# Kernel tuning notes

Measured on AMD Instinct MI355X. Metric: run time of the kernel, lower is better.

The kernel has to match this reference:

```python
import jax, jax.numpy as jnp
import numpy as np

EPS = 1e-5
NH, NP = 12, 4  # heads, points per level


def _ln(x, g, b):
    m = x.mean(-1, keepdims=True)
    v = x.var(-1, keepdims=True)
    return (x - m) / jnp.sqrt(v + EPS) * g + b


def _bilinear(v, g, H_, W_):
    # v: [B, nh, H_*W_, d] flattened feature map; g: [B, nh, Lq, np, 2] normalized locs in [0,1]
    # torch grid_sample(align_corners=False, padding='zeros') with grid = 2*loc-1 => pixel = loc*W - 0.5
    x = g[..., 0] * W_ - 0.5
    y = g[..., 1] * H_ - 0.5
    x0 = jnp.floor(x)
    y0 = jnp.floor(y)
    wx1 = x - x0
    wy1 = y - y0
    wx0 = 1.0 - wx1
    wy0 = 1.0 - wy1
    d = v.shape[-1]
    Bn, nh, Lq, np_ = x.shape
    out = jnp.zeros((Bn, nh, Lq, np_, d), v.dtype)
    for xi, yi, w in ((x0, y0, wx0 * wy0), (x0 + 1, y0, wx1 * wy0),
                      (x0, y0 + 1, wx0 * wy1), (x0 + 1, y0 + 1, wx1 * wy1)):
        valid = (xi >= 0) & (xi < W_) & (yi >= 0) & (yi < H_)
        xc = jnp.clip(xi, 0, W_ - 1).astype(jnp.int32)
        yc = jnp.clip(yi, 0, H_ - 1).astype(jnp.int32)
        idx = (yc * W_ + xc).reshape(Bn, nh, Lq * np_, 1)
        gv = jnp.take_along_axis(v, idx, axis=2).reshape(Bn, nh, Lq, np_, d)
        out = out + (w * valid.astype(v.dtype))[..., None] * gv
    return out


def setup_inputs() -> dict:
    key = jax.random.key(0)
    ks = jax.random.split(key, 16)
    B, Lq, C = 4, 4096, 768
    nl = 1
    Hs = Ws = 64
    Lin = Hs * Ws
    hid = int(C * 0.25)
    s = 0.02
    f32 = jnp.float32
    return {
        'query': jax.random.normal(ks[0], (B, Lq, C), f32),
        'reference_points': jax.random.uniform(ks[1], (B, Lq, nl, 2), f32),
        'feat': jax.random.normal(ks[2], (B, Lin, C), f32),
        'spatial_shapes': np.array([[Hs, Ws]], dtype=np.int64),
        'level_start_index': np.array([0], dtype=np.int64),
        'H': Hs, 'W': Ws,
        'qn_g': jnp.ones(C, f32), 'qn_b': jnp.zeros(C, f32),
        'fn_g': jnp.ones(C, f32), 'fn_b': jnp.zeros(C, f32),
        'Wv': jax.random.normal(ks[3], (C, C), f32) * s, 'bv': jnp.zeros(C, f32),
        'Woff': jax.random.normal(ks[4], (C, NH * nl * NP * 2), f32) * s,
        'boff': jax.random.normal(ks[5], (NH * nl * NP * 2,), f32) * 0.1,
        'Watt': jax.random.normal(ks[6], (C, NH * nl * NP), f32) * s,
        'batt': jnp.zeros(NH * nl * NP, f32),
        'Wout': jax.random.normal(ks[7], (C, C), f32) * s, 'bout': jnp.zeros(C, f32),
        'ffn_g': jnp.ones(C, f32), 'ffn_b': jnp.zeros(C, f32),
        'W1': jax.random.normal(ks[8], (C, hid), f32) * s, 'b1': jnp.zeros(hid, f32),
        'W2': jax.random.normal(ks[9], (hid, C), f32) * s, 'b2': jnp.zeros(C, f32),
    }


def reference(query, reference_points, feat, spatial_shapes, level_start_index, H, W,
              qn_g, qn_b, fn_g, fn_b, Wv, bv, Woff, boff, Watt, batt, Wout, bout,
              ffn_g, ffn_b, W1, b1, W2, b2):
    B, Lq, C = query.shape
    nl = spatial_shapes.shape[0]
    d = C // NH
    qn = _ln(query, qn_g, qn_b)
    fn = _ln(feat, fn_g, fn_b)
    value = (fn @ Wv + bv).reshape(B, -1, NH, d)
    off = (qn @ Woff + boff).reshape(B, Lq, NH, nl, NP, 2)
    attw = jax.nn.softmax((qn @ Watt + batt).reshape(B, Lq, NH, nl * NP), axis=-1)
    attw = attw.reshape(B, Lq, NH, nl, NP)
    # offset normalizer is [W_l, H_l]
    norm = np.stack([spatial_shapes[:, 1], spatial_shapes[:, 0]], -1).astype(np.float32)
    loc = reference_points[:, :, None, :, None, :] + off / jnp.asarray(norm)[None, None, None, :, None, :]
    out = jnp.zeros((B, NH, Lq, d), query.dtype)
    for l in range(nl):
        H_, W_ = int(spatial_shapes[l, 0]), int(spatial_shapes[l, 1])
        s0 = int(level_start_index[l])
        v = value[:, s0:s0 + H_ * W_].transpose(0, 2, 1, 3)       # [B, nh, HW, d]
        g = loc[:, :, :, l].transpose(0, 2, 1, 3, 4)              # [B, nh, Lq, np, 2]
        sampled = _bilinear(v, g, H_, W_)                         # [B, nh, Lq, np, d]
        w = attw[:, :, :, l].transpose(0, 2, 1, 3)                # [B, nh, Lq, np]
        out = out + jnp.sum(sampled * w[..., None], axis=3)
    attn = out.transpose(0, 2, 1, 3).reshape(B, Lq, C) @ Wout + bout
    query = query + attn
    h = _ln(query, ffn_g, ffn_b)
    h = jax.nn.gelu(h @ W1 + b1, approximate=False)
    return query + (h @ W2 + b2)
```

## Files before the change

### kernel.cpp

```cpp
#include <hip/hip_runtime.h>
#include <hip/hip_bf16.h>
#include <math.h>

#define B_    4
#define LQ    4096
#define CC    768
#define NH_   12
#define DH    64
#define NP_   4
#define HH    64
#define WW    64
#define HID   192
#define ROWS  (B_ * LQ)
#define EPS_  1e-5f

typedef __bf16 bf16x8 __attribute__((ext_vector_type(8)));
typedef __bf16 bf16x4 __attribute__((ext_vector_type(4)));
typedef float  f32x4  __attribute__((ext_vector_type(4)));

typedef __attribute__((address_space(3))) void* lds_vp;
typedef const __attribute__((address_space(1))) void* gbl_vp;

struct PrepJob { const float* W; __bf16* Wt; int K; int N; int Npad; };
struct PrepJobs { PrepJob j[6]; };

__global__ __launch_bounds__(256)
void prep_all(PrepJobs jobs) {
    PrepJob job = jobs.j[blockIdx.z];
    int k0 = blockIdx.x * 64, n0 = blockIdx.y * 64;
    if (k0 >= job.K || n0 >= job.Npad) return;
    __shared__ float tile[64][65];
    int c = threadIdx.x & 63, r0 = threadIdx.x >> 6;
    #pragma unroll
    for (int i = 0; i < 16; ++i) {
        int kk = i * 4 + r0;
        float v = 0.f;
        if (k0 + kk < job.K && n0 + c < job.N) v = job.W[(size_t)(k0 + kk) * job.N + n0 + c];
        tile[kk][c] = v;
    }
    __syncthreads();
    #pragma unroll
    for (int i = 0; i < 16; ++i) {
        int nn = i * 4 + r0;
        if (n0 + nn < job.Npad && k0 + c < job.K)
            job.Wt[(size_t)(n0 + nn) * job.K + k0 + c] = (__bf16)tile[c][nn];
    }
}

__inline__ __device__ float wave_sum64(float v) {
    #pragma unroll
    for (int o = 32; o > 0; o >>= 1) v += __shfl_down(v, o, 64);
    return v;
}

__global__ __launch_bounds__(256)
void ln2_kernel(const float* __restrict__ x0, const float* __restrict__ g0,
                const float* __restrict__ b0, __bf16* __restrict__ y0,
                const float* __restrict__ x1, const float* __restrict__ g1,
                const float* __restrict__ b1, __bf16* __restrict__ y1) {
    int sel = blockIdx.y;
    const float* x = sel ? x1 : x0;
    const float* g = sel ? g1 : g0;
    const float* b = sel ? b1 : b0;
    __bf16* y = sel ? y1 : y0;
    int row = blockIdx.x;
    const float* xr = x + (size_t)row * CC;
    __bf16* yr = y + (size_t)row * CC;
    int t = threadIdx.x;
    f32x4 xv = {0.f, 0.f, 0.f, 0.f};
    if (t < 192) xv = *(const f32x4*)(xr + t * 4);
    float s  = xv[0] + xv[1] + xv[2] + xv[3];
    float s2 = xv[0]*xv[0] + xv[1]*xv[1] + xv[2]*xv[2] + xv[3]*xv[3];
    __shared__ float red[8];
    float ws = wave_sum64(s), ws2 = wave_sum64(s2);
    int w = t >> 6;
    if ((t & 63) == 0) { red[w] = ws; red[4 + w] = ws2; }
    __syncthreads();
    float S  = red[0] + red[1] + red[2] + red[3];
    float S2 = red[4] + red[5] + red[6] + red[7];
    float mean = S / CC;
    float inv  = rsqrtf(S2 / CC - mean * mean + EPS_);
    if (t < 192) {
        f32x4 gv = *(const f32x4*)(g + t * 4);
        f32x4 bv = *(const f32x4*)(b + t * 4);
        bf16x4 o;
        #pragma unroll
        for (int e = 0; e < 4; ++e)
            o[e] = (__bf16)((xv[e] - mean) * inv * gv[e] + bv[e]);
        *(bf16x4*)(yr + t * 4) = o;
    }
}

__global__ __launch_bounds__(256)
void ln_bf_kernel(const __bf16* __restrict__ x, const float* __restrict__ g,
                  const float* __restrict__ b, __bf16* __restrict__ y) {
    int row = blockIdx.x;
    const __bf16* xr = x + (size_t)row * CC;
    __bf16* yr = y + (size_t)row * CC;
    int t = threadIdx.x;
    float xv[8]; bf16x8 raw = {};
    if (t < 96) raw = *(const bf16x8*)(xr + t * 8);
    float s = 0.f, s2 = 0.f;
    #pragma unroll
    for (int e = 0; e < 8; ++e) { xv[e] = (float)raw[e]; s += xv[e]; s2 += xv[e]*xv[e]; }
    __shared__ float red[8];
    float ws = wave_sum64(s), ws2 = wave_sum64(s2);
    int w = t >> 6;
    if ((t & 63) == 0) { red[w] = ws; red[4 + w] = ws2; }
    __syncthreads();
    float S  = red[0] + red[1] + red[2] + red[3];
    float S2 = red[4] + red[5] + red[6] + red[7];
    float mean = S / CC;
    float inv  = rsqrtf(S2 / CC - mean * mean + EPS_);
    if (t < 96) {
        bf16x8 o;
        #pragma unroll
        for (int e = 0; e < 8; ++e)
            o[e] = (__bf16)((xv[e] - mean) * inv * g[t * 8 + e] + b[t * 8 + e]);
        *(bf16x8*)(yr + t * 8) = o;
    }
}

__global__ __launch_bounds__(256, 8)
void gemm64(const __bf16* __restrict__ A, const __bf16* __restrict__ Bt,
            const float* __restrict__ ba, int Nsplit, const float* __restrict__ bb,
            const void* __restrict__ res, void* __restrict__ out,
            int M, int K, int N, int flags) {
    __shared__ __bf16 As[2][64 * 32];
    __shared__ __bf16 Bs[2][64 * 32];

    int t = threadIdx.x;
    int lane = t & 63, wave = t >> 6;

    int nwg = gridDim.x * gridDim.y;
    int bid = blockIdx.y * gridDim.x + blockIdx.x;
    int swz = (bid & 7) * (nwg >> 3) + (bid >> 3);
    int bx = swz % gridDim.x, by = swz / gridDim.x;
    int bm = by * 64, bn = bx * 64;

    f32x4 acc[4] = {};

    int row0 = t >> 2, kc0 = (t & 3) ^ ((row0 >> 1) & 3);
    const __bf16* a0 = A  + (size_t)(bm + row0) * K + kc0 * 8;
    const __bf16* b0 = Bt + (size_t)(bn + row0) * K + kc0 * 8;

    int rbase = wave * 16 + (lane & 15);
    int nbase = lane & 15;
    int kq = lane >> 4;

    #define STAGE(bi, kt) do {                                                                   \
        int koff_ = (kt) * 32;                                                                   \
        __builtin_amdgcn_global_load_lds((gbl_vp)(a0 + koff_), (lds_vp)&As[bi][t * 8], 16, 0, 0); \
        __builtin_amdgcn_global_load_lds((gbl_vp)(b0 + koff_), (lds_vp)&Bs[bi][t * 8], 16, 0, 0); \
    } while (0)

    #define COMPUTE(bi) do {                                                                     \
        bf16x8 afr = *(const bf16x8*)&As[bi][rbase * 32 + ((kq ^ ((rbase >> 1) & 3)) * 8)];      \
        _Pragma("unroll")                                                                        \
        for (int j = 0; j < 4; ++j) {                                                            \
            int n = nbase + j * 16;                                                              \
            bf16x8 bfr = *(const bf16x8*)&Bs[bi][n * 32 + ((kq ^ ((n >> 1) & 3)) * 8)];          \
            acc[j] = __builtin_amdgcn_mfma_f32_16x16x32_bf16(afr, bfr, acc[j], 0, 0, 0);         \
        }                                                                                        \
    } while (0)

    int nt = K >> 5;
    STAGE(0, 0);
    STAGE(1, 1);
    for (int tt = 0; tt < nt; ++tt) {
        int cur = tt & 1;
        if (tt < nt - 1) asm volatile("s_waitcnt vmcnt(2)\n\ts_barrier" ::: "memory");
        else             asm volatile("s_waitcnt vmcnt(0)\n\ts_barrier" ::: "memory");
        COMPUTE(cur);
        asm volatile("s_waitcnt lgkmcnt(0)\n\ts_barrier" ::: "memory");
        if (tt + 2 < nt) STAGE(cur, tt + 2);
    }

    #undef STAGE
    #undef COMPUTE

    int rowq = lane >> 4;
    int do_gelu = flags & 1, out_bf = flags & 2, res_bf = flags & 4;
    #pragma unroll
    for (int j = 0; j < 4; ++j) {
        int c = bn + j * 16 + (lane & 15);
        if (c < N) {
            float bias = (c < Nsplit) ? ba[c] : bb[c - Nsplit];
            #pragma unroll
            for (int r = 0; r < 4; ++r) {
                int m = bm + wave * 16 + rowq * 4 + r;
                float v = acc[j][r] + bias;
                if (do_gelu) v = 0.5f * v * (1.f + erff(v * 0.70710678118f));
                size_t oi = (size_t)m * N + c;
                if (res) v += res_bf ? (float)((const __bf16*)res)[oi]
                                     : ((const float*)res)[oi];
                if (out_bf) ((__bf16*)out)[oi] = (__bf16)v;
                else        ((float*)out)[oi]  = v;
            }
        }
    }
}

__global__ __launch_bounds__(256)
void sample_kernel(const __bf16* __restrict__ value, const float* __restrict__ offatt,
                   const float* __restrict__ refp, __bf16* __restrict__ out) {
    int wid  = blockIdx.x * 4 + (threadIdx.x >> 6);
    int lane = threadIdx.x & 63;
    int h  = wid % NH_;
    int bq = wid / NH_;
    int b  = bq / LQ;

    const float* oa = offatt + (size_t)bq * 144;
    float rx = refp[(size_t)bq * 2 + 0] * (float)WW - 0.5f;
    float ry = refp[(size_t)bq * 2 + 1] * (float)HH - 0.5f;

    float l0 = oa[96 + h * 4 + 0], l1 = oa[96 + h * 4 + 1];
    float l2 = oa[96 + h * 4 + 2], l3 = oa[96 + h * 4 + 3];
    float mx = fmaxf(fmaxf(l0, l1), fmaxf(l2, l3));
    float e0 = __expf(l0 - mx), e1 = __expf(l1 - mx);
    float e2 = __expf(l2 - mx), e3 = __expf(l3 - mx);
    float rs = 1.f / (e0 + e1 + e2 + e3);

    int pp = lane >> 4;
    int g  = lane & 15;
    float wpl = (pp == 0) ? e0 : (pp == 1) ? e1 : (pp == 2) ? e2 : e3;
    wpl *= rs;

    const float* oxy = oa + h * 8 + pp * 2;
    float x = rx + oxy[0];
    float y = ry + oxy[1];
    float x0f = floorf(x), y0f = floorf(y);
    float wx1 = x - x0f, wy1 = y - y0f;
    float wx0 = 1.f - wx1, wy0 = 1.f - wy1;
    int x0 = (int)x0f, y0 = (int)y0f;
    int x1 = x0 + 1, y1 = y0 + 1;
    float mx0 = ((unsigned)x0 < (unsigned)WW) ? wx0 : 0.f;
    float mx1 = ((unsigned)x1 < (unsigned)WW) ? wx1 : 0.f;
    float my0 = (((unsigned)y0 < (unsigned)HH) ? wy0 : 0.f) * wpl;
    float my1 = (((unsigned)y1 < (unsigned)HH) ? wy1 : 0.f) * wpl;
    int xc0 = x0 & (WW - 1), xc1 = x1 & (WW - 1);
    int r0 = (y0 & (HH - 1)) << 6, r1 = (y1 & (HH - 1)) << 6;

    const __bf16* vbase = value + (size_t)b * (LQ * CC) + h * DH + g * 4;
    bf16x4 v00 = *(const bf16x4*)(vbase + (size_t)(r0 + xc0) * CC);
    bf16x4 v01 = *(const bf16x4*)(vbase + (size_t)(r0 + xc1) * CC);
    bf16x4 v10 = *(const bf16x4*)(vbase + (size_t)(r1 + xc0) * CC);
    bf16x4 v11 = *(const bf16x4*)(vbase + (size_t)(r1 + xc1) * CC);
    float w00 = mx0 * my0, w01 = mx1 * my0, w10 = mx0 * my1, w11 = mx1 * my1;

    f32x4 acc;
    #pragma unroll
    for (int e = 0; e < 4; ++e)
        acc[e] = w00 * (float)v00[e] + w01 * (float)v01[e]
               + w10 * (float)v10[e] + w11 * (float)v11[e];

    #pragma unroll
    for (int e = 0; e < 4; ++e) {
        acc[e] += __shfl_xor(acc[e], 16, 64);
        acc[e] += __shfl_xor(acc[e], 32, 64);
    }
    if (pp == 0) {
        bf16x4 o;
        o[0] = (__bf16)acc[0]; o[1] = (__bf16)acc[1];
        o[2] = (__bf16)acc[2]; o[3] = (__bf16)acc[3];
        *(bf16x4*)(out + (size_t)bq * CC + h * DH + g * 4) = o;
    }
}

extern "C" void kernel_launch(void* const* d_in, const int* in_sizes, int n_in,
                              void* d_out, int out_size, void* d_ws, size_t ws_size,
                              hipStream_t stream) {
    const float* query = (const float*)d_in[0];
    const float* refp  = (const float*)d_in[1];
    const float* feat  = (const float*)d_in[2];
    const float* qn_g  = (const float*)d_in[7];
    const float* qn_b  = (const float*)d_in[8];
    const float* fn_g  = (const float*)d_in[9];
    const float* fn_b  = (const float*)d_in[10];
    const float* Wv    = (const float*)d_in[11];
    const float* bv    = (const float*)d_in[12];
    const float* Woff  = (const float*)d_in[13];
    const float* boff  = (const float*)d_in[14];
    const float* Watt  = (const float*)d_in[15];
    const float* batt  = (const float*)d_in[16];
    const float* Wout  = (const float*)d_in[17];
    const float* bout  = (const float*)d_in[18];
    const float* ffn_g = (const float*)d_in[19];
    const float* ffn_b = (const float*)d_in[20];
    const float* W1    = (const float*)d_in[21];
    const float* b1    = (const float*)d_in[22];
    const float* W2    = (const float*)d_in[23];
    const float* b2    = (const float*)d_in[24];
    float* out = (float*)d_out;

    char* ws = (char*)d_ws;
    __bf16* WvT    = (__bf16*)(ws + 0);
    __bf16* WcombT = (__bf16*)(ws + 1179648);
    __bf16* WoutT  = (__bf16*)(ws + 1572864);
    __bf16* W1T    = (__bf16*)(ws + 2752512);
    __bf16* W2T    = (__bf16*)(ws + 3145728);
    float*  offatt_f = (float*)(ws + 3670016);
    __bf16* h1_bf    = (__bf16*)offatt_f;
    __bf16* bufA     = (__bf16*)(ws + 13107200);
    __bf16* qn_bf    = bufA;
    __bf16* value_bf = bufA;
    __bf16* bufB     = (__bf16*)(ws + 38273024);
    __bf16* fn_bf    = bufB;
    __bf16* samp_bf  = bufB;
    __bf16* h_bf     = bufB;
    __bf16* attn_bf  = (__bf16*)(ws + 63438848);

    dim3 blk(256);

    PrepJobs jobs;
    jobs.j[0] = {Wv,   WvT,             768, 768, 768};
    jobs.j[1] = {Woff, WcombT,          768,  96,  96};
    jobs.j[2] = {Watt, WcombT + 96*768, 768,  48,  96};
    jobs.j[3] = {Wout, WoutT,           768, 768, 768};
    jobs.j[4] = {W1,   W1T,             768, 192, 192};
    jobs.j[5] = {W2,   W2T,             192, 768, 768};
    prep_all<<<dim3(12, 12, 6), blk, 0, stream>>>(jobs);

    ln2_kernel<<<dim3(ROWS, 2), blk, 0, stream>>>(query, qn_g, qn_b, qn_bf,
                                                  feat,  fn_g, fn_b, fn_bf);

    gemm64<<<dim3(3, ROWS / 64), blk, 0, stream>>>(
        qn_bf, WcombT, boff, 96, batt, nullptr, offatt_f, ROWS, CC, 144, 0);
    gemm64<<<dim3(12, ROWS / 64), blk, 0, stream>>>(
        fn_bf, WvT, bv, CC, nullptr, nullptr, value_bf, ROWS, CC, CC, 2);
    sample_kernel<<<ROWS * NH_ / 4, blk, 0, stream>>>(value_bf, offatt_f, refp, samp_bf);
    gemm64<<<dim3(12, ROWS / 64), blk, 0, stream>>>(
        samp_bf, WoutT, bout, CC, nullptr, query, attn_bf, ROWS, CC, CC, 2);
    ln_bf_kernel<<<ROWS, blk, 0, stream>>>(attn_bf, ffn_g, ffn_b, h_bf);
    gemm64<<<dim3(3, ROWS / 64), blk, 0, stream>>>(
        h_bf, W1T, b1, HID, nullptr, nullptr, h1_bf, ROWS, CC, HID, 1 | 2);
    gemm64<<<dim3(12, ROWS / 64), blk, 0, stream>>>(
        h1_bf, W2T, b2, CC, nullptr, attn_bf, out, ROWS, HID, CC, 4);
}
```

Measured before the change: 431.4 us.

## Replace LDS double-buffered GEMM with direct global-to-register MFMA operand loads

The GEMM no longer stages A and B tiles through shared memory with async global-to-LDS copies and barriers. Each wave now loads its MFMA fragments straight from global memory into registers, and the K loop is unrolled. This removes LDS traffic and barrier synchronisation. In exchange, the four waves each re-read the shared B tile from global memory or cache, the loads are strided 16-byte accesses per row, and the occupancy hint drops from 8 to 4 blocks.

```diff
diff --git a/kernel.cpp b/kernel.cpp
--- a/kernel.cpp
+++ b/kernel.cpp
@@ -17,9 +17,6 @@
 typedef __bf16 bf16x8 __attribute__((ext_vector_type(8)));
 typedef __bf16 bf16x4 __attribute__((ext_vector_type(4)));
 typedef float  f32x4  __attribute__((ext_vector_type(4)));
-
-typedef __attribute__((address_space(3))) void* lds_vp;
-typedef const __attribute__((address_space(1))) void* gbl_vp;
 
 struct PrepJob { const float* W; __bf16* Wt; int K; int N; int Npad; };
 struct PrepJobs { PrepJob j[6]; };
@@ -121,14 +118,11 @@
     }
 }
 
-__global__ __launch_bounds__(256, 8)
-void gemm64(const __bf16* __restrict__ A, const __bf16* __restrict__ Bt,
-            const float* __restrict__ ba, int Nsplit, const float* __restrict__ bb,
-            const void* __restrict__ res, void* __restrict__ out,
-            int M, int K, int N, int flags) {
-    __shared__ __bf16 As[2][64 * 32];
-    __shared__ __bf16 Bs[2][64 * 32];
-
+__global__ __launch_bounds__(256, 4)
+void gemm_reg(const __bf16* __restrict__ A, const __bf16* __restrict__ Bt,
+              const float* __restrict__ ba, int Nsplit, const float* __restrict__ bb,
+              const void* __restrict__ res, void* __restrict__ out,
+              int M, int K, int N, int flags) {
     int t = threadIdx.x;
     int lane = t & 63, wave = t >> 6;
 
@@ -138,52 +132,34 @@
     int bx = swz % gridDim.x, by = swz / gridDim.x;
     int bm = by * 64, bn = bx * 64;
 
+    int rsel = lane & 15, kq = lane >> 4;
+
+    const __bf16* pA  = A  + (size_t)(bm + wave * 16 + rsel) * K + kq * 8;
+    const __bf16* pB0 = Bt + (size_t)(bn + rsel)      * K + kq * 8;
+    const __bf16* pB1 = pB0 + (size_t)16 * K;
+    const __bf16* pB2 = pB0 + (size_t)32 * K;
+    const __bf16* pB3 = pB0 + (size_t)48 * K;
+
     f32x4 acc[4] = {};
 
-    int row0 = t >> 2, kc0 = (t & 3) ^ ((row0 >> 1) & 3);
-    const __bf16* a0 = A  + (size_t)(bm + row0) * K + kc0 * 8;
-    const __bf16* b0 = Bt + (size_t)(bn + row0) * K + kc0 * 8;
-
-    int rbase = wave * 16 + (lane & 15);
-    int nbase = lane & 15;
-    int kq = lane >> 4;
-
-    #define STAGE(bi, kt) do {                                                                   \
-        int koff_ = (kt) * 32;                                                                   \
-        __builtin_amdgcn_global_load_lds((gbl_vp)(a0 + koff_), (lds_vp)&As[bi][t * 8], 16, 0, 0); \
-        __builtin_amdgcn_global_load_lds((gbl_vp)(b0 + koff_), (lds_vp)&Bs[bi][t * 8], 16, 0, 0); \
-    } while (0)
-
-    #define COMPUTE(bi) do {                                                                     \
-        bf16x8 afr = *(const bf16x8*)&As[bi][rbase * 32 + ((kq ^ ((rbase >> 1) & 3)) * 8)];      \
-        _Pragma("unroll")                                                                        \
-        for (int j = 0; j < 4; ++j) {                                                            \
-            int n = nbase + j * 16;                                                              \
-            bf16x8 bfr = *(const bf16x8*)&Bs[bi][n * 32 + ((kq ^ ((n >> 1) & 3)) * 8)];          \
-            acc[j] = __builtin_amdgcn_mfma_f32_16x16x32_bf16(afr, bfr, acc[j], 0, 0, 0);         \
-        }                                                                                        \
-    } while (0)
-
-    int nt = K >> 5;
-    STAGE(0, 0);
-    STAGE(1, 1);
-    for (int tt = 0; tt < nt; ++tt) {
-        int cur = tt & 1;
-        if (tt < nt - 1) asm volatile("s_waitcnt vmcnt(2)\n\ts_barrier" ::: "memory");
-        else             asm volatile("s_waitcnt vmcnt(0)\n\ts_barrier" ::: "memory");
-        COMPUTE(cur);
-        asm volatile("s_waitcnt lgkmcnt(0)\n\ts_barrier" ::: "memory");
-        if (tt + 2 < nt) STAGE(cur, tt + 2);
-    }
-
-    #undef STAGE
-    #undef COMPUTE
+    #pragma unroll 6
+    for (int k0 = 0; k0 < K; k0 += 32) {
+        bf16x8 afr = *(const bf16x8*)(pA  + k0);
+        bf16x8 b0  = *(const bf16x8*)(pB0 + k0);
+        bf16x8 b1  = *(const bf16x8*)(pB1 + k0);
+        bf16x8 b2  = *(const bf16x8*)(pB2 + k0);
+        bf16x8 b3  = *(const bf16x8*)(pB3 + k0);
+        acc[0] = __builtin_amdgcn_mfma_f32_16x16x32_bf16(afr, b0, acc[0], 0, 0, 0);
+        acc[1] = __builtin_amdgcn_mfma_f32_16x16x32_bf16(afr, b1, acc[1], 0, 0, 0);
+        acc[2] = __builtin_amdgcn_mfma_f32_16x16x32_bf16(afr, b2, acc[2], 0, 0, 0);
+        acc[3] = __builtin_amdgcn_mfma_f32_16x16x32_bf16(afr, b3, acc[3], 0, 0, 0);
+    }
 
     int rowq = lane >> 4;
     int do_gelu = flags & 1, out_bf = flags & 2, res_bf = flags & 4;
     #pragma unroll
     for (int j = 0; j < 4; ++j) {
-        int c = bn + j * 16 + (lane & 15);
+        int c = bn + j * 16 + rsel;
         if (c < N) {
             float bias = (c < Nsplit) ? ba[c] : bb[c - Nsplit];
             #pragma unroll
@@ -324,16 +300,16 @@
     ln2_kernel<<<dim3(ROWS, 2), blk, 0, stream>>>(query, qn_g, qn_b, qn_bf,
                                                   feat,  fn_g, fn_b, fn_bf);
 
-    gemm64<<<dim3(3, ROWS / 64), blk, 0, stream>>>(
+    gemm_reg<<<dim3(3, ROWS / 64), blk, 0, stream>>>(
         qn_bf, WcombT, boff, 96, batt, nullptr, offatt_f, ROWS, CC, 144, 0);
-    gemm64<<<dim3(12, ROWS / 64), blk, 0, stream>>>(
+    gemm_reg<<<dim3(12, ROWS / 64), blk, 0, stream>>>(
         fn_bf, WvT, bv, CC, nullptr, nullptr, value_bf, ROWS, CC, CC, 2);
     sample_kernel<<<ROWS * NH_ / 4, blk, 0, stream>>>(value_bf, offatt_f, refp, samp_bf);
-    gemm64<<<dim3(12, ROWS / 64), blk, 0, stream>>>(
+    gemm_reg<<<dim3(12, ROWS / 64), blk, 0, stream>>>(
         samp_bf, WoutT, bout, CC, nullptr, query, attn_bf, ROWS, CC, CC, 2);
     ln_bf_kernel<<<ROWS, blk, 0, stream>>>(attn_bf, ffn_g, ffn_b, h_bf);
-    gemm64<<<dim3(3, ROWS / 64), blk, 0, stream>>>(
+    gemm_reg<<<dim3(3, ROWS / 64), blk, 0, stream>>>(
         h_bf, W1T, b1, HID, nullptr, nullptr, h1_bf, ROWS, CC, HID, 1 | 2);
-    gemm64<<<dim3(12, ROWS / 64), blk, 0, stream>>>(
+    gemm_reg<<<dim3(12, ROWS / 64), blk, 0, stream>>>(
         h1_bf, W2T, b2, CC, nullptr, attn_bf, out, ROWS, HID, CC, 4);
 }
```

Measured after the change: 736.8 us. +70.8%, slower.

## Add 256x256-tile GEMM kernel for the three wide N=768 projections

Applied to the files above, without the earlier changes.

Adds a 512-thread GEMM with 256x256 output tiles, 64-wide K steps, XOR-swizzled LDS layout and direct global-to-LDS loads. It replaces the 64x64-tile kernel for the value, output and second FFN projections. Larger tiles give more operand reuse per loaded byte and less global traffic. The trade-off is far fewer workgroups (192 per GEMM), which can leave CUs idle, plus heavy register and LDS use. The small GEMM drops its unused residual path and reorders its epilogue loops.

```diff
diff --git a/kernel.cpp b/kernel.cpp
--- a/kernel.cpp
+++ b/kernel.cpp
@@ -121,6 +121,107 @@
     }
 }
 
+__global__ __launch_bounds__(512, 2)
+void gemm256(const __bf16* __restrict__ A, const __bf16* __restrict__ Bt,
+             const float* __restrict__ ba, const void* __restrict__ res,
+             void* __restrict__ out, int M, int K, int N, int flags) {
+    __shared__ __bf16 As[2][256 * 64];
+    __shared__ __bf16 Bs[2][256 * 64];
+
+    int t = threadIdx.x;
+    int lane = t & 63, wave = t >> 6;
+
+    int nwg = gridDim.x * gridDim.y;
+    int bid = blockIdx.y * gridDim.x + blockIdx.x;
+    int swz = (bid & 7) * (nwg >> 3) + (bid >> 3);
+    int bx = swz % gridDim.x, by = swz / gridDim.x;
+    int bm = by * 256, bn = bx * 256;
+
+    int wm = wave >> 2, wn = wave & 3;
+    int rsel = lane & 15, kq = lane >> 4;
+
+    f32x4 acc[8][4] = {};
+
+    int srow = t >> 3, p = t & 7;
+    const __bf16* aS[4]; const __bf16* bS[4];
+    #pragma unroll
+    for (int i = 0; i < 4; ++i) {
+        int r = srow + 64 * i;
+        int c = p ^ ((r >> 1) & 7);
+        aS[i] = A  + (size_t)(bm + r) * K + c * 8;
+        bS[i] = Bt + (size_t)(bn + r) * K + c * 8;
+    }
+
+    #define STAGE(bi, kt) do {                                                                  \
+        int ko_ = (kt) * 64;                                                                    \
+        _Pragma("unroll")                                                                       \
+        for (int i = 0; i < 4; ++i) {                                                           \
+            __builtin_amdgcn_global_load_lds((gbl_vp)(aS[i] + ko_),                             \
+                (lds_vp)&As[bi][t * 8 + i * 4096], 16, 0, 0);                                   \
+            __builtin_amdgcn_global_load_lds((gbl_vp)(bS[i] + ko_),                             \
+                (lds_vp)&Bs[bi][t * 8 + i * 4096], 16, 0, 0);                                   \
+        }                                                                                       \
+    } while (0)
+
+    #define COMPUTE(bi) do {                                                                    \
+        _Pragma("unroll")                                                                       \
+        for (int h = 0; h < 2; ++h) {                                                           \
+            bf16x8 afr[8], bfr[4];                                                              \
+            _Pragma("unroll")                                                                   \
+            for (int i = 0; i < 8; ++i) {                                                       \
+                int r = wm * 128 + rsel + i * 16;                                               \
+                afr[i] = *(const bf16x8*)&As[bi][r * 64 + (((h * 4 + kq) ^ ((r >> 1) & 7)) * 8)]; \
+            }                                                                                   \
+            _Pragma("unroll")                                                                   \
+            for (int j = 0; j < 4; ++j) {                                                       \
+                int n = wn * 64 + rsel + j * 16;                                                \
+                bfr[j] = *(const bf16x8*)&Bs[bi][n * 64 + (((h * 4 + kq) ^ ((n >> 1) & 7)) * 8)]; \
+            }                                                                                   \
+            _Pragma("unroll")                                                                   \
+            for (int i = 0; i < 8; ++i)                                                         \
+                _Pragma("unroll")                                                               \
+                for (int j = 0; j < 4; ++j)                                                     \
+                    acc[i][j] = __builtin_amdgcn_mfma_f32_16x16x32_bf16(afr[i], bfr[j], acc[i][j], 0, 0, 0); \
+        }                                                                                       \
+    } while (0)
+
+    int nt = K >> 6;
+    STAGE(0, 0);
+    STAGE(1, 1);
+    for (int tt = 0; tt < nt; ++tt) {
+        int cur = tt & 1;
+        if (tt < nt - 1) asm volatile("s_waitcnt vmcnt(8)\n\ts_barrier" ::: "memory");
+        else             asm volatile("s_waitcnt vmcnt(0)\n\ts_barrier" ::: "memory");
+        COMPUTE(cur);
+        asm volatile("s_waitcnt lgkmcnt(0)\n\ts_barrier" ::: "memory");
+        if (tt + 2 < nt) STAGE(cur, tt + 2);
+    }
+
+    #undef STAGE
+    #undef COMPUTE
+
+    int rowq = lane >> 4;
+    int out_bf = flags & 2, res_bf = flags & 4;
+    #pragma unroll
+    for (int j = 0; j < 4; ++j) {
+        int c = bn + wn * 64 + j * 16 + rsel;
+        float bias = ba[c];
+        #pragma unroll
+        for (int i = 0; i < 8; ++i) {
+            #pragma unroll
+            for (int r = 0; r < 4; ++r) {
+                int m = bm + wm * 128 + i * 16 + rowq * 4 + r;
+                float v = acc[i][j][r] + bias;
+                size_t oi = (size_t)m * N + c;
+                if (res) v += res_bf ? (float)((const __bf16*)res)[oi]
+                                     : ((const float*)res)[oi];
+                if (out_bf) ((__bf16*)out)[oi] = (__bf16)v;
+                else        ((float*)out)[oi]  = v;
+            }
+        }
+    }
+}
+
 __global__ __launch_bounds__(256, 8)
 void gemm64(const __bf16* __restrict__ A, const __bf16* __restrict__ Bt,
             const float* __restrict__ ba, int Nsplit, const float* __restrict__ bb,
@@ -180,20 +281,17 @@
     #undef COMPUTE
 
     int rowq = lane >> 4;
-    int do_gelu = flags & 1, out_bf = flags & 2, res_bf = flags & 4;
-    #pragma unroll
-    for (int j = 0; j < 4; ++j) {
-        int c = bn + j * 16 + (lane & 15);
-        if (c < N) {
-            float bias = (c < Nsplit) ? ba[c] : bb[c - Nsplit];
-            #pragma unroll
-            for (int r = 0; r < 4; ++r) {
-                int m = bm + wave * 16 + rowq * 4 + r;
-                float v = acc[j][r] + bias;
+    int do_gelu = flags & 1, out_bf = flags & 2;
+    #pragma unroll
+    for (int r = 0; r < 4; ++r) {
+        int m = bm + wave * 16 + rowq * 4 + r;
+        #pragma unroll
+        for (int j = 0; j < 4; ++j) {
+            int c = bn + j * 16 + (lane & 15);
+            if (c < N) {
+                float v = acc[j][r] + ((c < Nsplit) ? ba[c] : bb[c - Nsplit]);
                 if (do_gelu) v = 0.5f * v * (1.f + erff(v * 0.70710678118f));
                 size_t oi = (size_t)m * N + c;
-                if (res) v += res_bf ? (float)((const __bf16*)res)[oi]
-                                     : ((const float*)res)[oi];
                 if (out_bf) ((__bf16*)out)[oi] = (__bf16)v;
                 else        ((float*)out)[oi]  = v;
             }
@@ -326,14 +424,14 @@
 
     gemm64<<<dim3(3, ROWS / 64), blk, 0, stream>>>(
         qn_bf, WcombT, boff, 96, batt, nullptr, offatt_f, ROWS, CC, 144, 0);
-    gemm64<<<dim3(12, ROWS / 64), blk, 0, stream>>>(
-        fn_bf, WvT, bv, CC, nullptr, nullptr, value_bf, ROWS, CC, CC, 2);
+    gemm256<<<dim3(3, ROWS / 256), dim3(512), 0, stream>>>(
+        fn_bf, WvT, bv, nullptr, value_bf, ROWS, CC, CC, 2);
     sample_kernel<<<ROWS * NH_ / 4, blk, 0, stream>>>(value_bf, offatt_f, refp, samp_bf);
-    gemm64<<<dim3(12, ROWS / 64), blk, 0, stream>>>(
-        samp_bf, WoutT, bout, CC, nullptr, query, attn_bf, ROWS, CC, CC, 2);
+    gemm256<<<dim3(3, ROWS / 256), dim3(512), 0, stream>>>(
+        samp_bf, WoutT, bout, query, attn_bf, ROWS, CC, CC, 2);
     ln_bf_kernel<<<ROWS, blk, 0, stream>>>(attn_bf, ffn_g, ffn_b, h_bf);
     gemm64<<<dim3(3, ROWS / 64), blk, 0, stream>>>(
         h_bf, W1T, b1, HID, nullptr, nullptr, h1_bf, ROWS, CC, HID, 1 | 2);
-    gemm64<<<dim3(12, ROWS / 64), blk, 0, stream>>>(
-        h1_bf, W2T, b2, CC, nullptr, attn_bf, out, ROWS, HID, CC, 4);
-}
+    gemm256<<<dim3(3, ROWS / 256), dim3(512), 0, stream>>>(
+        h1_bf, W2T, b2, attn_bf, out, ROWS, HID, CC, 4);
+}
```

After: 469.9 us. 1.09x slower.
